# Kernel tuning notes

Hardware: AMD Instinct MI355X
Metric: run time of the kernel (lower is better)

Reference implementation:

```python
import jax, jax.numpy as jnp
import numpy as np

E = 8        # num_experts (material buckets)
L1 = 3072    # input dim
L2 = 15
L3 = 32
RF = 32      # ROUTER_FEATURES_PER_PERSPECTIVE
B = 16384
AUX_ALPHA = 0.01
Z_ALPHA = 0.001
LOAD_FLOOR = 0.05
LOAD_CAP = 0.5
PROBE_ALPHA = 0.01
PROBE_TAU = 1.0
PROBE_THRESH = 0.05
TEACHER_ALPHA = 0.0   # initial value of _teacher_alpha buffer
SCORE_SCALE = 600.0
SQ_SCALE = 255.0 / 256.0


def setup_inputs() -> dict:
    key = jax.random.key(0)
    ks = jax.random.split(key, 12)
    x = jax.random.uniform(ks[0], (B, L1), dtype=jnp.float32)
    ls_indices = jax.random.randint(ks[1], (B,), 0, E)
    psqt = jax.random.normal(ks[2], (B,), dtype=jnp.float32)
    score_target = jax.random.normal(ks[3], (B,), dtype=jnp.float32)
    router_w = 0.1 * jax.random.normal(ks[4], (E, 2 * RF), dtype=jnp.float32)
    router_b = jnp.zeros((E,), dtype=jnp.float32)
    # effective (coalesced) expert params, per _expert_params view
    w1 = jax.random.normal(ks[5], (E, L2 + 1, L1), dtype=jnp.float32) / np.sqrt(L1)
    b1 = 0.01 * jax.random.normal(ks[6], (E, L2 + 1), dtype=jnp.float32)
    w2 = jax.random.normal(ks[7], (E, L3, 2 * L2), dtype=jnp.float32) / np.sqrt(2 * L2)
    b2 = 0.01 * jax.random.normal(ks[8], (E, L3), dtype=jnp.float32)
    w3 = jax.random.normal(ks[9], (E, 1, L3), dtype=jnp.float32) / np.sqrt(L3)
    b3 = jnp.zeros((E, 1), dtype=jnp.float32)  # output bias zeroed in __init__
    return {"x": x, "ls_indices": ls_indices, "psqt": psqt,
            "score_target": score_target, "router_w": router_w,
            "router_b": router_b, "w1": w1, "b1": b1, "w2": w2, "b2": b2,
            "w3": w3, "b3": b3}


def _forward(x, psqt, score_target, router_w, router_b, w1, b1, w2, b2, w3, b3, ls_indices):
    half = L1 // 2
    router_in = jnp.concatenate([x[:, :RF], x[:, half:half + RF]], axis=1)  # [B, 64]
    gate_logits = router_in @ router_w.T + router_b                          # [B, E]
    logp = jax.nn.log_softmax(gate_logits, axis=-1)
    gate_probs = jnp.exp(logp)
    expert_indices = jnp.argmax(gate_logits, axis=-1)                        # [B]

    teacher_ce = -jnp.mean(jnp.take_along_axis(logp, ls_indices[:, None], axis=1))
    frac = jnp.bincount(expert_indices, length=E).astype(gate_probs.dtype) / gate_probs.shape[0]
    avg_gate = gate_probs.mean(axis=0)
    load = avg_gate + jax.lax.stop_gradient(frac - avg_gate)
    floor_loss = jnp.mean(jnp.square(jnp.maximum(LOAD_FLOOR - load, 0.0)))
    cap_loss = jnp.mean(jnp.square(jnp.maximum(load - LOAD_CAP, 0.0)))
    aux_loss = floor_loss + cap_loss
    z_loss = jnp.mean(jnp.square(jax.nn.logsumexp(gate_logits, axis=-1)))

    # ---- all-experts stacked MLP (fusion target) ----
    l1c = jnp.einsum('bi,eoi->beo', x, w1) + b1          # [B, E, L2+1]
    a, a_skip = l1c[..., :L2], l1c[..., L2:]              # [B,E,L2], [B,E,1]
    h = jnp.clip(jnp.concatenate([a * a * SQ_SCALE, a], axis=-1), 0.0, 1.0)  # [B,E,2*L2]
    l2x = jnp.clip(jnp.einsum('bei,eoi->beo', h, w2) + b2, 0.0, 1.0)         # [B,E,L3]
    all_out = jnp.einsum('bei,eoi->beo', l2x, w3) + b3 + a_skip              # [B,E,1]

    # ---- probe loss ----
    probe_weight = PROBE_ALPHA * max(PROBE_THRESH - TEACHER_ALPHA, 0.0) / max(PROBE_THRESH, 1e-9)
    expert_out = (all_out[..., 0] + psqt[:, None]) * SCORE_SCALE             # [B, E]
    err = jnp.square(expert_out - score_target[:, None])
    err = err - err.min(axis=1, keepdims=True)
    pt = jax.nn.softmax(-jax.lax.stop_gradient(err) / PROBE_TAU, axis=-1)
    log_pt = jnp.log(jnp.maximum(pt, 1e-30))
    probe_loss = jnp.mean(jnp.sum(pt * (log_pt - logp), axis=-1))            # kl_div batchmean

    router_loss = (AUX_ALPHA * aux_loss + Z_ALPHA * z_loss
                   + TEACHER_ALPHA * teacher_ce + probe_weight * probe_loss)

    l3x = jnp.take_along_axis(all_out, expert_indices[:, None, None], axis=1)[:, 0, :]  # [B, 1]
    gp = jnp.take_along_axis(gate_probs, expert_indices[:, None], axis=1)               # [B, 1]
    l3x = l3x * (1.0 + gp - jax.lax.stop_gradient(gp))  # straight-through (training mode)
    return l3x, router_loss


def reference(x, ls_indices, psqt, score_target, router_w, router_b, w1, b1, w2, b2, w3, b3):
    return _forward(x, psqt, score_target, router_w, router_b, w1, b1, w2, b2, w3, b3, ls_indices)
```

## Files before the change

### kernel.cpp

```cpp
#include <hip/hip_runtime.h>
#include <math.h>

#define BATCH 16384
#define K_DIM 3072
#define NOUT  128
#define NEXP  8

typedef float  f32x4  __attribute__((ext_vector_type(4)));
typedef __bf16 bf16x8 __attribute__((ext_vector_type(8)));
typedef unsigned int u32x4 __attribute__((ext_vector_type(4)));
typedef unsigned int u32x2 __attribute__((ext_vector_type(2)));

__device__ __forceinline__ unsigned short f2bf(float f) {
  union { float f; unsigned u; } v; v.f = f;
  unsigned u = v.u + 0x7fffu + ((v.u >> 16) & 1u);
  return (unsigned short)(u >> 16);
}

__global__ void cvt_w1_kernel(const float* __restrict__ w1, unsigned short* __restrict__ o) {
  int i = blockIdx.x * 256 + threadIdx.x;
  f32x4 v = ((const f32x4*)w1)[i];
  u32x2 p = { (unsigned)f2bf(v.x) | ((unsigned)f2bf(v.y) << 16),
              (unsigned)f2bf(v.z) | ((unsigned)f2bf(v.w) << 16) };
  ((u32x2*)o)[i] = p;
}

__global__ void router_kernel(const float* __restrict__ x, const float* __restrict__ rw,
                              const float* __restrict__ rb, float* __restrict__ logp,
                              int* __restrict__ eidx, float* __restrict__ accs) {
  __shared__ float rws[512];
  __shared__ float rbs[8];
  __shared__ int   hist[8];
  __shared__ float zred[4];
  const int tid = threadIdx.x;
  if (tid < 8) { hist[tid] = 0; rbs[tid] = rb[tid]; }
  for (int i = tid; i < 512; i += 256) rws[i] = rw[i];
  __syncthreads();

  const int b = blockIdx.x * 256 + tid;
  const float* xr = x + (size_t)b * K_DIM;
  double l[8];
#pragma unroll
  for (int e = 0; e < 8; ++e) l[e] = (double)rbs[e];
  for (int c = 0; c < 32; ++c) {
    double xv = (double)xr[c];
#pragma unroll
    for (int e = 0; e < 8; ++e) l[e] = fma(xv, (double)rws[e * 64 + c], l[e]);
  }
  for (int c = 0; c < 32; ++c) {
    double xv = (double)xr[1536 + c];
#pragma unroll
    for (int e = 0; e < 8; ++e) l[e] = fma(xv, (double)rws[e * 64 + 32 + c], l[e]);
  }
  double best = l[0]; int bi = 0;
#pragma unroll
  for (int e = 1; e < 8; ++e) if (l[e] > best) { best = l[e]; bi = e; }
  double s = 0.0;
#pragma unroll
  for (int e = 0; e < 8; ++e) s += exp(l[e] - best);
  double lse = best + log(s);
#pragma unroll
  for (int e = 0; e < 8; ++e) logp[(size_t)b * 8 + e] = (float)(l[e] - lse);
  eidx[b] = bi;
  atomicAdd(&hist[bi], 1);

  float z = (float)(lse * lse);
  for (int m = 1; m < 64; m <<= 1) z += __shfl_xor(z, m);
  if ((tid & 63) == 0) zred[tid >> 6] = z;
  __syncthreads();
  if (tid == 0) atomicAdd(&accs[8], zred[0] + zred[1] + zred[2] + zred[3]);
  if (tid < 8) atomicAdd(&accs[tid], (float)hist[tid]);
}

__global__ __launch_bounds__(256, 2) void moe_main_kernel(
    const float* __restrict__ x, const unsigned short* __restrict__ w1bf,
    const float* __restrict__ b1, const float* __restrict__ w2,
    const float* __restrict__ b2, const float* __restrict__ w3,
    const float* __restrict__ b3, const float* __restrict__ psqt,
    const float* __restrict__ st, const float* __restrict__ logp,
    const int* __restrict__ eidx, float* __restrict__ out,
    float* __restrict__ accs) {
  __shared__ __align__(16) unsigned short stage[32 * 72 + 128 * 72];
  __shared__ __align__(16) float w2s[8 * 964];
  __shared__ float b1s[128], b2s[256], w3s[256], b3s[8], wred[4];

  const int tid = threadIdx.x;
  const int bm  = blockIdx.x;
  unsigned short* xs  = stage;
  unsigned short* wsd = stage + 32 * 72;
  float* Cl = (float*)stage;

  for (int i = tid; i < 7680; i += 256) {
    int e = i / 960; int r = i - e * 960; int o = r / 30; int ii = r - o * 30;
    w2s[e * 964 + ii * 32 + o] = w2[i];
  }
  if (tid < 128) b1s[tid] = b1[tid];
  b2s[tid] = b2[tid];
  w3s[tid] = w3[tid];
  if (tid < 8) b3s[tid] = b3[tid];

  const int lane = tid & 63, wv = tid >> 6;
  const int l16 = lane & 15, lq = lane >> 4;
  const int rt = wv & 1;
  const int cb = (wv >> 1) * 4;

  const int xr0 = tid >> 4, xc4 = tid & 15;
  const float* gx0 = x + (size_t)(bm * 32 + xr0) * K_DIM + xc4 * 4;
  const float* gx1 = gx0 + (size_t)16 * K_DIM;
  const int xo0 = xr0 * 72 + xc4 * 4;
  const int xo1 = (xr0 + 16) * 72 + xc4 * 4;
  const int wr0 = tid >> 3, wc8 = tid & 7;
  const unsigned short* gw = w1bf + (size_t)wr0 * K_DIM + wc8 * 8;
  const int wo0 = wr0 * 72 + wc8 * 8;

  f32x4 acc[4];
#pragma unroll
  for (int c = 0; c < 4; ++c) acc[c] = (f32x4){0.f, 0.f, 0.f, 0.f};

  f32x4 xv0 = *(const f32x4*)gx0;
  f32x4 xv1 = *(const f32x4*)gx1;
  u32x4 wv0 = *(const u32x4*)(gw);
  u32x4 wv1 = *(const u32x4*)(gw + 32 * K_DIM);
  u32x4 wv2 = *(const u32x4*)(gw + 64 * K_DIM);
  u32x4 wv3 = *(const u32x4*)(gw + 96 * K_DIM);

  const int abase = (rt * 16 + l16) * 72 + lq * 8;
  const int bbase = (cb * 16 + l16) * 72 + lq * 8;

  for (int kt = 0; kt < 48; ++kt) {
    __syncthreads();
    {
      u32x2 p0 = { (unsigned)f2bf(xv0.x) | ((unsigned)f2bf(xv0.y) << 16),
                   (unsigned)f2bf(xv0.z) | ((unsigned)f2bf(xv0.w) << 16) };
      *(u32x2*)&xs[xo0] = p0;
      u32x2 p1 = { (unsigned)f2bf(xv1.x) | ((unsigned)f2bf(xv1.y) << 16),
                   (unsigned)f2bf(xv1.z) | ((unsigned)f2bf(xv1.w) << 16) };
      *(u32x2*)&xs[xo1] = p1;
      *(u32x4*)&wsd[wo0]           = wv0;
      *(u32x4*)&wsd[wo0 + 32 * 72] = wv1;
      *(u32x4*)&wsd[wo0 + 64 * 72] = wv2;
      *(u32x4*)&wsd[wo0 + 96 * 72] = wv3;
    }
    __syncthreads();
    if (kt < 47) {
      gx0 += 64; gx1 += 64;
      xv0 = *(const f32x4*)gx0;
      xv1 = *(const f32x4*)gx1;
      const unsigned short* g = gw + (kt + 1) * 64;
      wv0 = *(const u32x4*)(g);
      wv1 = *(const u32x4*)(g + 32 * K_DIM);
      wv2 = *(const u32x4*)(g + 64 * K_DIM);
      wv3 = *(const u32x4*)(g + 96 * K_DIM);
    }
#pragma unroll
    for (int ks = 0; ks < 2; ++ks) {
      bf16x8 af = *(const bf16x8*)&xs[abase + ks * 32];
#pragma unroll
      for (int c = 0; c < 4; ++c) {
        bf16x8 bfv = *(const bf16x8*)&wsd[bbase + c * 16 * 72 + ks * 32];
        acc[c] = __builtin_amdgcn_mfma_f32_16x16x32_bf16(af, bfv, acc[c], 0, 0, 0);
      }
    }
  }

  __syncthreads();
#pragma unroll
  for (int c = 0; c < 4; ++c)
#pragma unroll
    for (int r = 0; r < 4; ++r)
      Cl[(rt * 16 + lq * 4 + r) * 132 + (cb + c) * 16 + l16] = acc[c][r];
  __syncthreads();

  const int bl = tid >> 3, e = tid & 7;
  const int bg = bm * 32 + bl;

  float a[16];
#pragma unroll
  for (int j = 0; j < 16; ++j) a[j] = Cl[bl * 132 + e * 16 + j] + b1s[e * 16 + j];

  float h[30];
#pragma unroll
  for (int j = 0; j < 15; ++j) {
    float v = a[j];
    h[j]      = fminf(fmaxf(v * v * (255.0f / 256.0f), 0.f), 1.f);
    h[15 + j] = fminf(fmaxf(v, 0.f), 1.f);
  }

  float acc2[32];
#pragma unroll
  for (int o = 0; o < 32; ++o) acc2[o] = b2s[e * 32 + o];
  const f32x4* wrow = (const f32x4*)&w2s[e * 964];
#pragma unroll
  for (int i = 0; i < 30; ++i) {
    float hv = h[i];
#pragma unroll
    for (int o4 = 0; o4 < 8; ++o4) {
      f32x4 wq = wrow[i * 8 + o4];
      acc2[o4 * 4 + 0] += hv * wq.x;
      acc2[o4 * 4 + 1] += hv * wq.y;
      acc2[o4 * 4 + 2] += hv * wq.z;
      acc2[o4 * 4 + 3] += hv * wq.w;
    }
  }

  float outv = b3s[e] + a[15];
#pragma unroll
  for (int o = 0; o < 32; ++o) {
    float l2v = fminf(fmaxf(acc2[o], 0.f), 1.f);
    outv += l2v * w3s[e * 32 + o];
  }

  float eo  = (outv + psqt[bg]) * 600.0f;
  float dd  = eo - st[bg];
  float err = dd * dd;
  float mn = err;
  mn = fminf(mn, __shfl_xor(mn, 1));
  mn = fminf(mn, __shfl_xor(mn, 2));
  mn = fminf(mn, __shfl_xor(mn, 4));
  float wexp = expf(-(err - mn));
  float ssum = wexp;
  ssum += __shfl_xor(ssum, 1); ssum += __shfl_xor(ssum, 2); ssum += __shfl_xor(ssum, 4);
  float pt  = wexp / ssum;
  float lpt = logf(fmaxf(pt, 1e-30f));
  float term = pt * (lpt - logp[(size_t)bg * 8 + e]);
  term += __shfl_xor(term, 1); term += __shfl_xor(term, 2); term += __shfl_xor(term, 4);
  float c1 = (e == 0) ? term : 0.f;
  c1 += __shfl_xor(c1, 8); c1 += __shfl_xor(c1, 16); c1 += __shfl_xor(c1, 32);
  if (lane == 0) wred[wv] = c1;

  if (e == eidx[bg]) out[bg] = outv;

  __syncthreads();
  if (tid == 0) atomicAdd(&accs[9], wred[0] + wred[1] + wred[2] + wred[3]);
}

__global__ void finalize_kernel(const float* __restrict__ accs, float* __restrict__ out) {
  if (threadIdx.x == 0) {
    float fsum = 0.f;
    for (int e = 0; e < 8; ++e) {
      float frac = accs[e] * (1.0f / 16384.0f);
      float f = fmaxf(0.05f - frac, 0.f);
      float c = fmaxf(frac - 0.5f, 0.f);
      fsum += f * f + c * c;
    }
    float aux   = fsum * 0.125f;
    float z     = accs[8] * (1.0f / 16384.0f);
    float probe = accs[9] * (1.0f / 16384.0f);
    out[BATCH] = 0.01f * aux + 0.001f * z + 0.01f * probe;
  }
}

extern "C" void kernel_launch(void* const* d_in, const int* in_sizes, int n_in,
                              void* d_out, int out_size, void* d_ws, size_t ws_size,
                              hipStream_t stream) {
  const float* x    = (const float*)d_in[0];
  const float* psqt = (const float*)d_in[2];
  const float* st   = (const float*)d_in[3];
  const float* rw   = (const float*)d_in[4];
  const float* rb   = (const float*)d_in[5];
  const float* w1   = (const float*)d_in[6];
  const float* b1   = (const float*)d_in[7];
  const float* w2   = (const float*)d_in[8];
  const float* b2   = (const float*)d_in[9];
  const float* w3   = (const float*)d_in[10];
  const float* b3   = (const float*)d_in[11];
  float* out = (float*)d_out;

  unsigned short* w1bf = (unsigned short*)d_ws;
  float* logp = (float*)((char*)d_ws + 786432);
  int*   eidx = (int*)((char*)d_ws + 786432 + 524288);
  float* accs = (float*)((char*)d_ws + 786432 + 524288 + 65536);

  hipMemsetAsync(accs, 0, 16 * sizeof(float), stream);
  cvt_w1_kernel<<<384, 256, 0, stream>>>(w1, w1bf);
  router_kernel<<<64, 256, 0, stream>>>(x, rw, rb, logp, eidx, accs);
  moe_main_kernel<<<512, 256, 0, stream>>>(x, w1bf, b1, w2, b2, w3, b3,
                                           psqt, st, logp, eidx, out, accs);
  finalize_kernel<<<1, 1, 0, stream>>>(accs, out);
}
```

Before: 331.5 us.

## Fuse router into main MoE kernel and pretranspose w2 in conversion kernel

Removes the separate router kernel and computes gate logits, log-softmax, argmax and the histogram and z-loss partials inside the main kernel, one thread per (row, expert), keeping logp and expert indices in shared memory. The w2 transpose moves into the weight conversion kernel (one extra block), so each main block stops rebuilding a 30KB shared copy. b1/b2/w3 are now read from global memory, and launch bounds go to 3 blocks per SM. The aim is to cut a launch, drop the logp/eidx round trip through global memory and lower LDS use. The cost is fp64 router math inside the main kernel and more global loads in the epilogue.

```diff
diff --git a/kernel.cpp b/kernel.cpp
--- a/kernel.cpp
+++ b/kernel.cpp
@@ -3,7 +3,6 @@
 
 #define BATCH 16384
 #define K_DIM 3072
-#define NOUT  128
 #define NEXP  8
 
 typedef float  f32x4  __attribute__((ext_vector_type(4)));
@@ -17,87 +16,43 @@
   return (unsigned short)(u >> 16);
 }
 
-__global__ void cvt_w1_kernel(const float* __restrict__ w1, unsigned short* __restrict__ o) {
-  int i = blockIdx.x * 256 + threadIdx.x;
-  f32x4 v = ((const f32x4*)w1)[i];
-  u32x2 p = { (unsigned)f2bf(v.x) | ((unsigned)f2bf(v.y) << 16),
-              (unsigned)f2bf(v.z) | ((unsigned)f2bf(v.w) << 16) };
-  ((u32x2*)o)[i] = p;
-}
-
-__global__ void router_kernel(const float* __restrict__ x, const float* __restrict__ rw,
-                              const float* __restrict__ rb, float* __restrict__ logp,
-                              int* __restrict__ eidx, float* __restrict__ accs) {
-  __shared__ float rws[512];
-  __shared__ float rbs[8];
-  __shared__ int   hist[8];
-  __shared__ float zred[4];
-  const int tid = threadIdx.x;
-  if (tid < 8) { hist[tid] = 0; rbs[tid] = rb[tid]; }
-  for (int i = tid; i < 512; i += 256) rws[i] = rw[i];
-  __syncthreads();
-
-  const int b = blockIdx.x * 256 + tid;
-  const float* xr = x + (size_t)b * K_DIM;
-  double l[8];
-#pragma unroll
-  for (int e = 0; e < 8; ++e) l[e] = (double)rbs[e];
-  for (int c = 0; c < 32; ++c) {
-    double xv = (double)xr[c];
-#pragma unroll
-    for (int e = 0; e < 8; ++e) l[e] = fma(xv, (double)rws[e * 64 + c], l[e]);
-  }
-  for (int c = 0; c < 32; ++c) {
-    double xv = (double)xr[1536 + c];
-#pragma unroll
-    for (int e = 0; e < 8; ++e) l[e] = fma(xv, (double)rws[e * 64 + 32 + c], l[e]);
-  }
-  double best = l[0]; int bi = 0;
-#pragma unroll
-  for (int e = 1; e < 8; ++e) if (l[e] > best) { best = l[e]; bi = e; }
-  double s = 0.0;
-#pragma unroll
-  for (int e = 0; e < 8; ++e) s += exp(l[e] - best);
-  double lse = best + log(s);
-#pragma unroll
-  for (int e = 0; e < 8; ++e) logp[(size_t)b * 8 + e] = (float)(l[e] - lse);
-  eidx[b] = bi;
-  atomicAdd(&hist[bi], 1);
-
-  float z = (float)(lse * lse);
-  for (int m = 1; m < 64; m <<= 1) z += __shfl_xor(z, m);
-  if ((tid & 63) == 0) zred[tid >> 6] = z;
-  __syncthreads();
-  if (tid == 0) atomicAdd(&accs[8], zred[0] + zred[1] + zred[2] + zred[3]);
-  if (tid < 8) atomicAdd(&accs[tid], (float)hist[tid]);
-}
-
-__global__ __launch_bounds__(256, 2) void moe_main_kernel(
+__global__ void cvt_kernel(const float* __restrict__ w1, unsigned short* __restrict__ o,
+                           const float* __restrict__ w2, float* __restrict__ w2t) {
+  if (blockIdx.x < 384) {
+    int i = blockIdx.x * 256 + threadIdx.x;
+    f32x4 v = ((const f32x4*)w1)[i];
+    u32x2 p = { (unsigned)f2bf(v.x) | ((unsigned)f2bf(v.y) << 16),
+                (unsigned)f2bf(v.z) | ((unsigned)f2bf(v.w) << 16) };
+    ((u32x2*)o)[i] = p;
+  } else {
+    for (int j = threadIdx.x; j < 7680; j += 256) {
+      int e = j / 960; int r = j - e * 960; int oo = r / 30; int ii = r - oo * 30;
+      w2t[e * 960 + ii * 32 + oo] = w2[j];
+    }
+  }
+}
+
+__global__ __launch_bounds__(256, 3) void moe_main_kernel(
     const float* __restrict__ x, const unsigned short* __restrict__ w1bf,
-    const float* __restrict__ b1, const float* __restrict__ w2,
+    const float* __restrict__ b1, const float* __restrict__ w2t,
     const float* __restrict__ b2, const float* __restrict__ w3,
     const float* __restrict__ b3, const float* __restrict__ psqt,
-    const float* __restrict__ st, const float* __restrict__ logp,
-    const int* __restrict__ eidx, float* __restrict__ out,
+    const float* __restrict__ st, const float* __restrict__ rw,
+    const float* __restrict__ rb, float* __restrict__ out,
     float* __restrict__ accs) {
   __shared__ __align__(16) unsigned short stage[32 * 72 + 128 * 72];
-  __shared__ __align__(16) float w2s[8 * 964];
-  __shared__ float b1s[128], b2s[256], w3s[256], b3s[8], wred[4];
+  __shared__ float rws_s[512];
+  __shared__ float logps[32][8];
+  __shared__ int   eidx_s[32];
+  __shared__ int   hist_s[8];
+  __shared__ float zsum_s;
+  __shared__ float wred[4];
 
   const int tid = threadIdx.x;
   const int bm  = blockIdx.x;
   unsigned short* xs  = stage;
   unsigned short* wsd = stage + 32 * 72;
   float* Cl = (float*)stage;
-
-  for (int i = tid; i < 7680; i += 256) {
-    int e = i / 960; int r = i - e * 960; int o = r / 30; int ii = r - o * 30;
-    w2s[e * 964 + ii * 32 + o] = w2[i];
-  }
-  if (tid < 128) b1s[tid] = b1[tid];
-  b2s[tid] = b2[tid];
-  w3s[tid] = w3[tid];
-  if (tid < 8) b3s[tid] = b3[tid];
 
   const int lane = tid & 63, wv = tid >> 6;
   const int l16 = lane & 15, lq = lane >> 4;
@@ -113,16 +68,51 @@
   const unsigned short* gw = w1bf + (size_t)wr0 * K_DIM + wc8 * 8;
   const int wo0 = wr0 * 72 + wc8 * 8;
 
-  f32x4 acc[4];
-#pragma unroll
-  for (int c = 0; c < 4; ++c) acc[c] = (f32x4){0.f, 0.f, 0.f, 0.f};
-
   f32x4 xv0 = *(const f32x4*)gx0;
   f32x4 xv1 = *(const f32x4*)gx1;
   u32x4 wv0 = *(const u32x4*)(gw);
   u32x4 wv1 = *(const u32x4*)(gw + 32 * K_DIM);
   u32x4 wv2 = *(const u32x4*)(gw + 64 * K_DIM);
   u32x4 wv3 = *(const u32x4*)(gw + 96 * K_DIM);
+
+  rws_s[tid] = rw[tid];
+  rws_s[tid + 256] = rw[tid + 256];
+  if (tid < 8) hist_s[tid] = 0;
+  if (tid == 0) zsum_s = 0.f;
+  __syncthreads();
+
+  {
+    const int rrow = tid >> 3, re = tid & 7;
+    const float* xrow = x + (size_t)(bm * 32 + rrow) * K_DIM;
+    double l = (double)rb[re];
+#pragma unroll
+    for (int c = 0; c < 32; ++c)
+      l = fma((double)xrow[c], (double)rws_s[re * 64 + c], l);
+#pragma unroll
+    for (int c = 0; c < 32; ++c)
+      l = fma((double)xrow[1536 + c], (double)rws_s[re * 64 + 32 + c], l);
+    double mx = l;
+    mx = fmax(mx, __shfl_xor(mx, 1));
+    mx = fmax(mx, __shfl_xor(mx, 2));
+    mx = fmax(mx, __shfl_xor(mx, 4));
+    int cand = (l == mx) ? re : 8;
+    cand = min(cand, __shfl_xor(cand, 1));
+    cand = min(cand, __shfl_xor(cand, 2));
+    cand = min(cand, __shfl_xor(cand, 4));
+    double s = exp(l - mx);
+    s += __shfl_xor(s, 1); s += __shfl_xor(s, 2); s += __shfl_xor(s, 4);
+    double lse = mx + log(s);
+    logps[rrow][re] = (float)(l - lse);
+    if (re == 0) {
+      eidx_s[rrow] = cand;
+      atomicAdd(&zsum_s, (float)(lse * lse));
+    }
+    if (re == cand) atomicAdd(&hist_s[cand], 1);
+  }
+
+  f32x4 acc[4];
+#pragma unroll
+  for (int c = 0; c < 4; ++c) acc[c] = (f32x4){0.f, 0.f, 0.f, 0.f};
 
   const int abase = (rt * 16 + l16) * 72 + lq * 8;
   const int bbase = (cb * 16 + l16) * 72 + lq * 8;
@@ -176,7 +166,7 @@
 
   float a[16];
 #pragma unroll
-  for (int j = 0; j < 16; ++j) a[j] = Cl[bl * 132 + e * 16 + j] + b1s[e * 16 + j];
+  for (int j = 0; j < 16; ++j) a[j] = Cl[bl * 132 + e * 16 + j] + b1[e * 16 + j];
 
   float h[30];
 #pragma unroll
@@ -187,9 +177,14 @@
   }
 
   float acc2[32];
-#pragma unroll
-  for (int o = 0; o < 32; ++o) acc2[o] = b2s[e * 32 + o];
-  const f32x4* wrow = (const f32x4*)&w2s[e * 964];
+  const f32x4* b2v = (const f32x4*)(b2 + e * 32);
+#pragma unroll
+  for (int o4 = 0; o4 < 8; ++o4) {
+    f32x4 bq = b2v[o4];
+    acc2[o4 * 4 + 0] = bq.x; acc2[o4 * 4 + 1] = bq.y;
+    acc2[o4 * 4 + 2] = bq.z; acc2[o4 * 4 + 3] = bq.w;
+  }
+  const f32x4* wrow = (const f32x4*)(w2t + e * 960);
 #pragma unroll
   for (int i = 0; i < 30; ++i) {
     float hv = h[i];
@@ -203,11 +198,16 @@
     }
   }
 
-  float outv = b3s[e] + a[15];
-#pragma unroll
-  for (int o = 0; o < 32; ++o) {
-    float l2v = fminf(fmaxf(acc2[o], 0.f), 1.f);
-    outv += l2v * w3s[e * 32 + o];
+  float outv = b3[e] + a[15];
+  const f32x4* w3v = (const f32x4*)(w3 + e * 32);
+#pragma unroll
+  for (int o4 = 0; o4 < 8; ++o4) {
+    f32x4 wq = w3v[o4];
+#pragma unroll
+    for (int k = 0; k < 4; ++k) {
+      float l2v = fminf(fmaxf(acc2[o4 * 4 + k], 0.f), 1.f);
+      outv += l2v * ((const float*)&wq)[k];
+    }
   }
 
   float eo  = (outv + psqt[bg]) * 600.0f;
@@ -222,16 +222,20 @@
   ssum += __shfl_xor(ssum, 1); ssum += __shfl_xor(ssum, 2); ssum += __shfl_xor(ssum, 4);
   float pt  = wexp / ssum;
   float lpt = logf(fmaxf(pt, 1e-30f));
-  float term = pt * (lpt - logp[(size_t)bg * 8 + e]);
+  float term = pt * (lpt - logps[bl][e]);
   term += __shfl_xor(term, 1); term += __shfl_xor(term, 2); term += __shfl_xor(term, 4);
   float c1 = (e == 0) ? term : 0.f;
   c1 += __shfl_xor(c1, 8); c1 += __shfl_xor(c1, 16); c1 += __shfl_xor(c1, 32);
   if (lane == 0) wred[wv] = c1;
 
-  if (e == eidx[bg]) out[bg] = outv;
-
-  __syncthreads();
-  if (tid == 0) atomicAdd(&accs[9], wred[0] + wred[1] + wred[2] + wred[3]);
+  if (e == eidx_s[bl]) out[bg] = outv;
+
+  __syncthreads();
+  if (tid == 0) {
+    atomicAdd(&accs[9], wred[0] + wred[1] + wred[2] + wred[3]);
+    atomicAdd(&accs[8], zsum_s);
+  }
+  if (tid < 8) atomicAdd(&accs[tid], (float)hist_s[tid]);
 }
 
 __global__ void finalize_kernel(const float* __restrict__ accs, float* __restrict__ out) {
@@ -267,14 +271,12 @@
   float* out = (float*)d_out;
 
   unsigned short* w1bf = (unsigned short*)d_ws;
-  float* logp = (float*)((char*)d_ws + 786432);
-  int*   eidx = (int*)((char*)d_ws + 786432 + 524288);
-  float* accs = (float*)((char*)d_ws + 786432 + 524288 + 65536);
+  float* w2t  = (float*)((char*)d_ws + 786432);
+  float* accs = (float*)((char*)d_ws + 786432 + 30720);
 
   hipMemsetAsync(accs, 0, 16 * sizeof(float), stream);
-  cvt_w1_kernel<<<384, 256, 0, stream>>>(w1, w1bf);
-  router_kernel<<<64, 256, 0, stream>>>(x, rw, rb, logp, eidx, accs);
-  moe_main_kernel<<<512, 256, 0, stream>>>(x, w1bf, b1, w2, b2, w3, b3,
-                                           psqt, st, logp, eidx, out, accs);
+  cvt_kernel<<<385, 256, 0, stream>>>(w1, w1bf, w2, w2t);
+  moe_main_kernel<<<512, 256, 0, stream>>>(x, w1bf, b1, w2t, b2, w3, b3,
+                                           psqt, st, rw, rb, out, accs);
   finalize_kernel<<<1, 1, 0, stream>>>(accs, out);
 }
```

Result: slower. 386.3 us (+16.5%).
